# Performance work log

Measured on AMD Instinct MI355X. Metric: run time of the kernel, lower is better.

## Reference

```python
import jax, jax.numpy as jnp
import numpy as np

EPS_MASK = 1e-9   # module fills masked scores with eps, NOT -inf
LN_EPS = 1e-5

def _layer_norm(x, g, b):
    mu = jnp.mean(x, axis=-1, keepdims=True)
    var = jnp.mean(jnp.square(x - mu), axis=-1, keepdims=True)
    return (x - mu) * jax.lax.rsqrt(var + LN_EPS) * g + b

def _mha(q_in, k_in, v_in, wq, bq, wk, bk, wv, bv, wo, bo, mask, nhead):
    B, Sq, D = q_in.shape
    dk = D // nhead
    def proj(x, w, b):
        y = x @ w + b                                   # [B,S,D]
        return y.reshape(B, -1, nhead, dk).transpose(0, 2, 1, 3)  # [B,h,S,dk]
    q, k, v = proj(q_in, wq, bq), proj(k_in, wk, bk), proj(v_in, wv, bv)
    scores = jnp.einsum('bhqd,bhkd->bhqk', q, k) / np.sqrt(dk).astype(q.dtype)
    if mask is not None:
        scores = jnp.where(mask[:, None, :, :] == 0, jnp.asarray(EPS_MASK, scores.dtype), scores)
    p = jax.nn.softmax(scores, axis=-1)                 # dropout = identity (eval)
    x = jnp.einsum('bhqk,bhkd->bhqd', p, v)
    x = x.transpose(0, 2, 1, 3).reshape(B, Sq, D)
    return x @ wo + bo

def _forward_post(tgt, memory, tgt_pos, memory_pos, tgt_mask, memory_mask, p):
    nhead = 8
    # self-attention (q=k=tgt+pos, v=tgt)
    q = tgt + tgt_pos
    sa = _mha(q, q, tgt, p['sa_wq'], p['sa_bq'], p['sa_wk'], p['sa_bk'],
              p['sa_wv'], p['sa_bv'], p['sa_wo'], p['sa_bo'], tgt_mask, nhead)
    tgt = _layer_norm(tgt + sa, p['ln1_g'], p['ln1_b'])
    # cross-attention (q=tgt+tgt_pos, k=memory+memory_pos, v=memory)
    mq = tgt + tgt_pos
    mk = memory + memory_pos
    ca = _mha(mq, mk, memory, p['ca_wq'], p['ca_bq'], p['ca_wk'], p['ca_bk'],
              p['ca_wv'], p['ca_bv'], p['ca_wo'], p['ca_bo'], memory_mask, nhead)
    tgt = _layer_norm(tgt + ca, p['ln2_g'], p['ln2_b'])
    # FFN
    h = jax.nn.relu(tgt @ p['mlp_w1'] + p['mlp_b1'])
    ff = h @ p['mlp_w2'] + p['mlp_b2']
    return _layer_norm(tgt + ff, p['ln3_g'], p['ln3_b'])

def setup_inputs() -> dict:
    key = jax.random.key(0)
    B, S, M, D, H = 4, 1024, 1024, 512, 2048
    ks = iter(jax.random.split(key, 40))
    d = {
        'tgt': jax.random.normal(next(ks), (B, S, D), jnp.float32),
        'memory': jax.random.normal(next(ks), (B, M, D), jnp.float32),
        'tgt_pos': jax.random.normal(next(ks), (B, S, D), jnp.float32),
        'memory_pos': jax.random.normal(next(ks), (B, M, D), jnp.float32),
        'tgt_mask': jax.random.randint(next(ks), (B, S, S), 0, 2, jnp.int32),
        'memory_mask': jax.random.randint(next(ks), (B, S, M), 0, 2, jnp.int32),
    }
    for pre in ('sa', 'ca'):
        for nm in ('q', 'k', 'v', 'o'):
            d[f'{pre}_w{nm}'] = jax.random.normal(next(ks), (D, D), jnp.float32) * 0.02
            d[f'{pre}_b{nm}'] = jnp.zeros((D,), jnp.float32)
    for i in (1, 2, 3):
        d[f'ln{i}_g'] = jnp.ones((D,), jnp.float32)
        d[f'ln{i}_b'] = jnp.zeros((D,), jnp.float32)
    d['mlp_w1'] = jax.random.normal(next(ks), (D, H), jnp.float32) * 0.02
    d['mlp_b1'] = jnp.zeros((H,), jnp.float32)
    d['mlp_w2'] = jax.random.normal(next(ks), (H, D), jnp.float32) * 0.02
    d['mlp_b2'] = jnp.zeros((D,), jnp.float32)
    return d

def reference(tgt, memory, tgt_pos, memory_pos, tgt_mask, memory_mask,
              sa_wq, sa_bq, sa_wk, sa_bk, sa_wv, sa_bv, sa_wo, sa_bo,
              ca_wq, ca_bq, ca_wk, ca_bk, ca_wv, ca_bv, ca_wo, ca_bo,
              ln1_g, ln1_b, ln2_g, ln2_b, ln3_g, ln3_b,
              mlp_w1, mlp_b1, mlp_w2, mlp_b2):
    p = dict(sa_wq=sa_wq, sa_bq=sa_bq, sa_wk=sa_wk, sa_bk=sa_bk, sa_wv=sa_wv,
             sa_bv=sa_bv, sa_wo=sa_wo, sa_bo=sa_bo, ca_wq=ca_wq, ca_bq=ca_bq,
             ca_wk=ca_wk, ca_bk=ca_bk, ca_wv=ca_wv, ca_bv=ca_bv, ca_wo=ca_wo,
             ca_bo=ca_bo, ln1_g=ln1_g, ln1_b=ln1_b, ln2_g=ln2_g, ln2_b=ln2_b,
             ln3_g=ln3_g, ln3_b=ln3_b, mlp_w1=mlp_w1, mlp_b1=mlp_b1,
             mlp_w2=mlp_w2, mlp_b2=mlp_b2)
    return _forward_post(tgt, memory, tgt_pos, memory_pos, tgt_mask, memory_mask, p)
```

## Files before the change

kernel.cpp:

```cpp
#include <hip/hip_runtime.h>
#include <stdint.h>

typedef unsigned int u32;
typedef unsigned long long u64;
typedef unsigned short u16;
typedef __attribute__((ext_vector_type(8))) __bf16 bf16x8;
typedef __attribute__((ext_vector_type(4))) float f32x4;

#define DEV __device__ __forceinline__

DEV u16 f2bf(float f) {
    u32 x = __builtin_bit_cast(u32, f);
    u32 r = (x + 0x7FFFu + ((x >> 16) & 1u)) >> 16;
    return (u16)r;
}

DEV float bf2f(u16 x) {
    u32 u = (u32)x << 16;
    return __builtin_bit_cast(float, u);
}

DEV void unp8(uint4 u, float* f) {
    f[0] = bf2f((u16)u.x); f[1] = bf2f((u16)(u.x >> 16));
    f[2] = bf2f((u16)u.y); f[3] = bf2f((u16)(u.y >> 16));
    f[4] = bf2f((u16)u.z); f[5] = bf2f((u16)(u.z >> 16));
    f[6] = bf2f((u16)u.w); f[7] = bf2f((u16)(u.w >> 16));
}

DEV bf16x8 ldg8(const u16* p) {
    return __builtin_bit_cast(bf16x8, *(const uint4*)p);
}

DEV u32 pk2(float a, float b) {
    return (u32)f2bf(a) | ((u32)f2bf(b) << 16);
}

DEV void g2l16(const u16* g, u16* l) {
    __builtin_amdgcn_global_load_lds(
        (const __attribute__((address_space(1))) u32*)g,
        (__attribute__((address_space(3))) u32*)l, 16, 0, 0);
}

DEV f32x4 mfma16(bf16x8 a, bf16x8 b, f32x4 c) {
    return __builtin_amdgcn_mfma_f32_16x16x32_bf16(a, b, c, 0, 0, 0);
}

struct ProArgs {
    const float* w[10];
    u16* wtbase;
    const float4 *tgt, *tpos, *mem, *mpos;
    ushort4 *qin, *tgtb, *memb, *mkb, *tposb;
    const int4 *m1, *m2;
    u32 *o1, *o2;
};
__global__ __launch_bounds__(256) void prologue_kernel(ProArgs a) {
    const int bx = blockIdx.x, t = threadIdx.x;
    if (bx < 10240) {
        int z = bx >> 10, bxx = bx & 1023;
        int Kd = (z == 9) ? 2048 : 512;
        int Nd = (z == 8) ? 2048 : 512;
        size_t off = (z < 8) ? (size_t)z * 262144
                             : (z == 8 ? (size_t)2097152 : (size_t)3145728);
        u16* out = a.wtbase + off;
        int nx = Nd / 32;
        int txile = bxx % nx, tyile = bxx / nx;
        if (tyile >= Kd / 32) return;
        const float* w = a.w[z];
        __shared__ float tl[32][33];
        int tx = t & 31, ty = t >> 5;
#pragma unroll
        for (int j = 0; j < 4; ++j)
            tl[ty + j * 8][tx] = w[(size_t)(tyile * 32 + ty + j * 8) * Nd + txile * 32 + tx];
        __syncthreads();
#pragma unroll
        for (int j = 0; j < 4; ++j)
            out[(size_t)(txile * 32 + ty + j * 8) * Kd + tyile * 32 + tx] = f2bf(tl[tx][ty + j * 8]);
    } else if (bx < 12288) {
        int i = (bx - 10240) * 256 + t;
        float4 tt = a.tgt[i], p = a.tpos[i], m = a.mem[i], mp = a.mpos[i];
        a.qin[i]  = make_ushort4(f2bf(tt.x + p.x), f2bf(tt.y + p.y), f2bf(tt.z + p.z), f2bf(tt.w + p.w));
        a.tgtb[i] = make_ushort4(f2bf(tt.x), f2bf(tt.y), f2bf(tt.z), f2bf(tt.w));
        a.memb[i] = make_ushort4(f2bf(m.x), f2bf(m.y), f2bf(m.z), f2bf(m.w));
        a.mkb[i]  = make_ushort4(f2bf(m.x + mp.x), f2bf(m.y + mp.y), f2bf(m.z + mp.z), f2bf(m.w + mp.w));
        a.tposb[i]= make_ushort4(f2bf(p.x), f2bf(p.y), f2bf(p.z), f2bf(p.w));
    } else {
        int i = (bx - 12288) * 256 + t;
        const int n8 = 524288;
        bool first = i < n8;
        int idx = first ? i : i - n8;
        const int4* src = first ? a.m1 : a.m2;
        int4 x = src[idx * 2], y = src[idx * 2 + 1];
        u32 by = (u32)(x.x != 0) | ((u32)(x.y != 0) << 1) | ((u32)(x.z != 0) << 2) |
                 ((u32)(x.w != 0) << 3) | ((u32)(y.x != 0) << 4) | ((u32)(y.y != 0) << 5) |
                 ((u32)(y.z != 0) << 6) | ((u32)(y.w != 0) << 7);
        u32 w = by | (__shfl_down(by, 1) << 8) | (__shfl_down(by, 2) << 16) |
                (__shfl_down(by, 3) << 24);
        if ((t & 3) == 0) (first ? a.o1 : a.o2)[idx >> 2] = w;
    }
}

struct GemmSet {
    const u16* A; const u16* W; const float* bias; void* out;
    float oscale; int epi; int k0; int klen;
};
struct GemmArgs5 { GemmSet s[5]; };

template <int BM, int BN>
__global__ __launch_bounds__(256) void gemm_kernel(GemmArgs5 args, int M, int N, int Kd) {
    constexpr int MF = BM / 32, NF = BN / 32;
    const GemmSet gs = args.s[blockIdx.z];
    const u16* __restrict__ A = gs.A;
    const u16* __restrict__ W = gs.W;
    const int t = threadIdx.x;
    const int lane = t & 63;
    const int g = lane >> 4, r16 = lane & 15;
    const int wave = t >> 6;
    const int wm = wave >> 1, wn = wave & 1;
    const int nwg = gridDim.x * gridDim.y;
    const int fid = blockIdx.y * gridDim.x + blockIdx.x;
    const int qq = nwg >> 3;
    const int lid = (fid & 7) * qq + (fid >> 3);
    const int m0 = (lid / gridDim.x) * BM, n0 = (lid % gridDim.x) * BN;

    __shared__ __align__(16) u16 As[BM * 64];
    __shared__ __align__(16) u16 Bs[BN * 64];

    f32x4 acc[MF][NF];
#pragma unroll
    for (int m = 0; m < MF; ++m)
#pragma unroll
        for (int n = 0; n < NF; ++n) acc[m][n] = f32x4{0.f, 0.f, 0.f, 0.f};

    const int kend = gs.k0 + gs.klen;
    for (int kk = gs.k0; kk < kend; kk += 64) {
        __syncthreads();
#pragma unroll
        for (int i = 0; i < BM / 32; ++i) {
            int cid = t + i * 256, row = cid >> 3, c = cid & 7;
            g2l16(A + (size_t)(m0 + row) * Kd + kk + ((c ^ (row & 7)) << 3), &As[cid << 3]);
        }
#pragma unroll
        for (int i = 0; i < BN / 32; ++i) {
            int cid = t + i * 256, row = cid >> 3, c = cid & 7;
            g2l16(W + (size_t)(n0 + row) * Kd + kk + ((c ^ (row & 7)) << 3), &Bs[cid << 3]);
        }
        __syncthreads();
#pragma unroll
        for (int ks = 0; ks < 2; ++ks) {
            bf16x8 af[MF], bfr[NF];
#pragma unroll
            for (int m = 0; m < MF; ++m) {
                int row = wm * (MF * 16) + m * 16 + r16;
                af[m] = *(const bf16x8*)&As[(row << 6) + (((ks * 4 + g) ^ (row & 7)) << 3)];
            }
#pragma unroll
            for (int n = 0; n < NF; ++n) {
                int row = wn * (NF * 16) + n * 16 + r16;
                bfr[n] = *(const bf16x8*)&Bs[(row << 6) + (((ks * 4 + g) ^ (row & 7)) << 3)];
            }
#pragma unroll
            for (int m = 0; m < MF; ++m)
#pragma unroll
                for (int n = 0; n < NF; ++n)
                    acc[m][n] = mfma16(af[m], bfr[n], acc[m][n]);
        }
    }
    const int epi = gs.epi;
#pragma unroll
    for (int m = 0; m < MF; ++m) {
        int row0 = m0 + wm * (MF * 16) + m * 16 + g * 4;
#pragma unroll
        for (int n = 0; n < NF; ++n) {
            int col = n0 + wn * (NF * 16) + n * 16 + r16;
            float bv = gs.bias ? gs.bias[col] : 0.f;
            float v[4];
#pragma unroll
            for (int r = 0; r < 4; ++r) v[r] = (acc[m][n][r] + bv) * gs.oscale;
            if (epi == 1) {
#pragma unroll
                for (int r = 0; r < 4; ++r) v[r] = fmaxf(v[r], 0.f);
            }
            if (epi == 3) {
                int bb = row0 >> 10, s = row0 & 1023;
                u16* o = (u16*)gs.out +
                         ((size_t)(bb * 8 + (col >> 6)) * 64 + (col & 63)) * 1024 + s;
                *(ushort4*)o = make_ushort4(f2bf(v[0]), f2bf(v[1]), f2bf(v[2]), f2bf(v[3]));
            } else {
                u16* o = (u16*)gs.out;
#pragma unroll
                for (int r = 0; r < 4; ++r) o[(size_t)(row0 + r) * N + col] = f2bf(v[r]);
            }
        }
    }
}

__global__ __launch_bounds__(512, 4) void attn_part_kernel(
    const u16* __restrict__ Q, const u16* __restrict__ K,
    const u16* __restrict__ VT, const u32* __restrict__ mb,
    u16* __restrict__ OP, float2* __restrict__ ML) {
    constexpr int Lq = 1024, Lk = 1024, NCH = 8;
    const int t = threadIdx.x, lane = t & 63, wave = t >> 6;
    const int g = lane >> 4, r16 = lane & 15;
    const int h = blockIdx.y;
    const int b = blockIdx.z >> 1, p = blockIdx.z & 1;
    const int bh = b * 8 + h;
    const int q0 = blockIdx.x * 128 + wave * 16;
    const int kc0 = p * (Lk >> 1);

    __shared__ __align__(16) u16 Ks[2][64][64];
    __shared__ __align__(16) u16 Vs[2][64][64];
    __shared__ __align__(16) u16 Pl[8][16][72];

    const size_t qrow = (size_t)b * Lq + q0 + r16;
    const u16* qp = Q + qrow * 512 + h * 64 + g * 8;
    bf16x8 qb0 = ldg8(qp), qb1 = ldg8(qp + 32);
    const u32* mrow = mb + qrow * (Lk >> 5);

    const int sid = t & 255;
    const bool isK = t < 256;
    const int s1 = sid, s2 = sid + 256;
    const int r1 = s1 >> 3, c1 = s1 & 7;
    const int r2 = s2 >> 3, c2 = s2 & 7;
    const u16 *sgA, *sgB;
    if (isK) {
        const u16* kbase = K + (size_t)b * Lk * 512 + h * 64;
        sgA = kbase + (size_t)(kc0 + r1) * 512 + ((c1 ^ (r1 & 7)) << 3);
        sgB = kbase + (size_t)(kc0 + r2) * 512 + ((c2 ^ (r2 & 7)) << 3);
    } else {
        const u16* vbase = VT + (size_t)bh * 64 * Lk + kc0;
        sgA = vbase + (size_t)r1 * Lk + ((c1 ^ (r1 & 7)) << 3);
        sgB = vbase + (size_t)r2 * Lk + ((c2 ^ (r2 & 7)) << 3);
    }
    const size_t adv = isK ? (size_t)64 * 512 : 64;
    u16* const base = isK ? &Ks[0][0][0] : &Vs[0][0][0];
    u16* const slA = base + s1 * 8;
    u16* const slB = base + s2 * 8;

    f32x4 acc[4];
#pragma unroll
    for (int dt = 0; dt < 4; ++dt) acc[dt] = f32x4{0.f, 0.f, 0.f, 0.f};
    float mrun = -INFINITY, lrun = 0.f;
    const f32x4 zf = {0.f, 0.f, 0.f, 0.f};

    g2l16(sgA, slA);
    g2l16(sgB, slB);
    __syncthreads();

#pragma unroll
    for (int c = 0; c < NCH; ++c) {
        const int buf = c & 1, nbuf = buf ^ 1;
        const int kc = kc0 + c * 64;
        if (c + 1 < NCH) {
            g2l16(sgA + (size_t)(c + 1) * adv, slA + nbuf * 4096);
            g2l16(sgB + (size_t)(c + 1) * adv, slB + nbuf * 4096);
        }
        const u16* kb = &Ks[buf][0][0];
        const u16* vb = &Vs[buf][0][0];
        f32x4 s[4];
#pragma unroll
        for (int j = 0; j < 4; ++j) {
            int row = j * 16 + r16;
            bf16x8 ka0 = *(const bf16x8*)(kb + row * 64 + ((g ^ (row & 7)) << 3));
            bf16x8 ka1 = *(const bf16x8*)(kb + row * 64 + (((4 + g) ^ (row & 7)) << 3));
            s[j] = mfma16(ka0, qb0, zf);
            s[j] = mfma16(ka1, qb1, s[j]);
        }
        u32 mw0 = mrow[kc >> 5], mw1 = mrow[(kc >> 5) + 1];
        float sv[16];
#pragma unroll
        for (int j = 0; j < 4; ++j) {
            u32 w = (j < 2) ? mw0 : mw1;
            int bbase = (16 * j) & 31;
#pragma unroll
            for (int r = 0; r < 4; ++r) {
                int bit = bbase + g * 4 + r;
                sv[4 * j + r] = ((w >> bit) & 1) ? s[j][r] : 1e-9f;
            }
        }
        float tm = fmaxf(fmaxf(fmaxf(sv[0], sv[1]), fmaxf(sv[2], sv[3])),
                         fmaxf(fmaxf(sv[4], sv[5]), fmaxf(sv[6], sv[7])));
        float tm2 = fmaxf(fmaxf(fmaxf(sv[8], sv[9]), fmaxf(sv[10], sv[11])),
                          fmaxf(fmaxf(sv[12], sv[13]), fmaxf(sv[14], sv[15])));
        tm = fmaxf(tm, tm2);
        tm = fmaxf(tm, __shfl_xor(tm, 16));
        tm = fmaxf(tm, __shfl_xor(tm, 32));
        if (!__all(tm <= mrun + 8.f)) {
            float mn = fmaxf(mrun, tm);
            float alpha = __expf(mrun - mn);
            mrun = mn;
            lrun *= alpha;
#pragma unroll
            for (int r = 0; r < 4; ++r) {
                float ar = __shfl(alpha, g * 4 + r);
#pragma unroll
                for (int dt = 0; dt < 4; ++dt) acc[dt][r] *= ar;
            }
        }
        float ts = 0.f;
#pragma unroll
        for (int j = 0; j < 16; ++j) { sv[j] = __expf(sv[j] - mrun); ts += sv[j]; }
        ts += __shfl_xor(ts, 16);
        ts += __shfl_xor(ts, 32);
        lrun += ts;

#pragma unroll
        for (int j = 0; j < 4; ++j) {
            uint2 u;
            u.x = pk2(sv[4 * j], sv[4 * j + 1]);
            u.y = pk2(sv[4 * j + 2], sv[4 * j + 3]);
            *(uint2*)&Pl[wave][r16][16 * j + g * 4] = u;
        }
        bf16x8 pf0 = *(const bf16x8*)&Pl[wave][r16][g * 8];
        bf16x8 pf1 = *(const bf16x8*)&Pl[wave][r16][32 + g * 8];
#pragma unroll
        for (int dt = 0; dt < 4; ++dt) {
            int row = dt * 16 + r16;
            bf16x8 vf0 = *(const bf16x8*)(vb + row * 64 + ((g ^ (row & 7)) << 3));
            bf16x8 vf1 = *(const bf16x8*)(vb + row * 64 + (((4 + g) ^ (row & 7)) << 3));
            acc[dt] = mfma16(pf0, vf0, acc[dt]);
            acc[dt] = mfma16(pf1, vf1, acc[dt]);
        }
        __syncthreads();
    }

    if (lane < 16)
        ML[(size_t)p * 32768 + (size_t)bh * 1024 + q0 + lane] = make_float2(mrun, lrun);
    const size_t obase = (size_t)p * 2097152 + ((size_t)bh * 1024 + q0) * 64;
#pragma unroll
    for (int dt = 0; dt < 4; ++dt)
#pragma unroll
        for (int r = 0; r < 4; ++r)
            OP[obase + (size_t)(g * 4 + r) * 64 + dt * 16 + r16] = f2bf(acc[dt][r]);
}

__global__ __launch_bounds__(256) void attn_combine_kernel(
    const u16* __restrict__ OP, const float2* __restrict__ ML, u16* __restrict__ O) {
    int gid = blockIdx.x * 256 + threadIdx.x;
    int row = gid >> 3, seg = gid & 7;
    size_t idx = (size_t)row * 64 + seg * 8;
    float2 ml0 = ML[row], ml1 = ML[32768 + row];
    float M = fmaxf(ml0.x, ml1.x);
    float w0 = __expf(ml0.x - M), w1 = __expf(ml1.x - M);
    float rden = 1.f / (ml0.y * w0 + ml1.y * w1);
    w0 *= rden; w1 *= rden;
    float a[8], b[8];
    unp8(*(const uint4*)(OP + idx), a);
    unp8(*(const uint4*)(OP + 2097152 + idx), b);
    int bh = row >> 10, q = row & 1023;
    int bb = bh >> 3, h = bh & 7;
    u16* o = O + ((size_t)(bb * 1024 + q)) * 512 + h * 64 + seg * 8;
    uint4 r;
    r.x = pk2(a[0] * w0 + b[0] * w1, a[1] * w0 + b[1] * w1);
    r.y = pk2(a[2] * w0 + b[2] * w1, a[3] * w0 + b[3] * w1);
    r.z = pk2(a[4] * w0 + b[4] * w1, a[5] * w0 + b[5] * w1);
    r.w = pk2(a[6] * w0 + b[6] * w1, a[7] * w0 + b[7] * w1);
    *(uint4*)o = r;
}

template <int MODE>
__global__ __launch_bounds__(256) void ln_kernel(
    const u16* __restrict__ a, const u16* __restrict__ b1, const u16* __restrict__ b2,
    const float* __restrict__ gam, const float* __restrict__ bet,
    const u16* __restrict__ pos,
    u16* __restrict__ yb, u16* __restrict__ qb, float* __restrict__ yf) {
    const int lane = threadIdx.x & 63;
    const int row = blockIdx.x * 4 + (threadIdx.x >> 6);
    const size_t base = (size_t)row * 512 + lane * 8;
    float av[8], bv[8], cv[8];
    unp8(*(const uint4*)(a + base), av);
    unp8(*(const uint4*)(b1 + base), bv);
    unp8(*(const uint4*)(b2 + base), cv);
    float x[8];
#pragma unroll
    for (int j = 0; j < 8; ++j) x[j] = av[j] + bv[j] + cv[j];
    float s1 = 0.f, s2 = 0.f;
#pragma unroll
    for (int j = 0; j < 8; ++j) { s1 += x[j]; s2 += x[j] * x[j]; }
#pragma unroll
    for (int d = 1; d < 64; d <<= 1) { s1 += __shfl_xor(s1, d); s2 += __shfl_xor(s2, d); }
    float mean = s1 * (1.f / 512.f);
    float var = s2 * (1.f / 512.f) - mean * mean;
    float rs = rsqrtf(var + 1e-5f);
    float4 gv0 = ((const float4*)(gam + lane * 8))[0];
    float4 gv1 = ((const float4*)(gam + lane * 8))[1];
    float4 be0 = ((const float4*)(bet + lane * 8))[0];
    float4 be1 = ((const float4*)(bet + lane * 8))[1];
    float gg[8] = {gv0.x, gv0.y, gv0.z, gv0.w, gv1.x, gv1.y, gv1.z, gv1.w};
    float bb[8] = {be0.x, be0.y, be0.z, be0.w, be1.x, be1.y, be1.z, be1.w};
    float y[8];
#pragma unroll
    for (int j = 0; j < 8; ++j) y[j] = (x[j] - mean) * rs * gg[j] + bb[j];
    if (MODE == 2) {
        ((float4*)(yf + base))[0] = make_float4(y[0], y[1], y[2], y[3]);
        ((float4*)(yf + base))[1] = make_float4(y[4], y[5], y[6], y[7]);
        return;
    }
    uint4 r;
    r.x = pk2(y[0], y[1]); r.y = pk2(y[2], y[3]);
    r.z = pk2(y[4], y[5]); r.w = pk2(y[6], y[7]);
    *(uint4*)(yb + base) = r;
    if (MODE == 0) {
        float pv[8];
        unp8(*(const uint4*)(pos + base), pv);
        uint4 q;
        q.x = pk2(y[0] + pv[0], y[1] + pv[1]);
        q.y = pk2(y[2] + pv[2], y[3] + pv[3]);
        q.z = pk2(y[4] + pv[4], y[5] + pv[5]);
        q.w = pk2(y[6] + pv[6], y[7] + pv[7]);
        *(uint4*)(qb + base) = q;
    }
}

extern "C" void kernel_launch(void* const* d_in, const int* in_sizes, int n_in,
                              void* d_out, int out_size, void* d_ws, size_t ws_size,
                              hipStream_t stream) {
    (void)in_sizes; (void)n_in; (void)out_size; (void)ws_size;
    const float* tgt      = (const float*)d_in[0];
    const float* memory   = (const float*)d_in[1];
    const float* tgt_pos  = (const float*)d_in[2];
    const float* mem_pos  = (const float*)d_in[3];
    const int*   tgt_mask = (const int*)d_in[4];
    const int*   mem_mask = (const int*)d_in[5];
    const float* sa_b[4] = {(const float*)d_in[7], (const float*)d_in[9],
                            (const float*)d_in[11], (const float*)d_in[13]};
    const float* ca_b[4] = {(const float*)d_in[15], (const float*)d_in[17],
                            (const float*)d_in[19], (const float*)d_in[21]};
    const float* ln1_g = (const float*)d_in[22]; const float* ln1_b = (const float*)d_in[23];
    const float* ln2_g = (const float*)d_in[24]; const float* ln2_b = (const float*)d_in[25];
    const float* ln3_g = (const float*)d_in[26]; const float* ln3_b = (const float*)d_in[27];
    const float* mlp_b1 = (const float*)d_in[29];
    const float* mlp_b2 = (const float*)d_in[31];

    const size_t MiB = 1024 * 1024;
    char* ws = (char*)d_ws;
    u16*  WT  = (u16*)(ws + 0);
    u32*  MBS = (u32*)(ws + 8 * MiB);
    u32*  MBC = (u32*)(ws + 8 * MiB + 512 * 1024);
    u16*  QIN = (u16*)(ws + 9 * MiB);
    u16*  TGTB= (u16*)(ws + 13 * MiB);
    u16*  MEMB= (u16*)(ws + 17 * MiB);
    u16*  MKB = (u16*)(ws + 21 * MiB);
    u16*  QM  = (u16*)(ws + 25 * MiB);
    u16*  KMS = (u16*)(ws + 29 * MiB);
    u16*  KMC = (u16*)(ws + 33 * MiB);
    u16*  VTS = (u16*)(ws + 37 * MiB);
    u16*  VTC = (u16*)(ws + 41 * MiB);
    u16*  ATNB= (u16*)(ws + 45 * MiB);
    u16*  P1B = (u16*)(ws + 49 * MiB);
    u16*  X1B = (u16*)(ws + 53 * MiB);
    u16*  MQB = (u16*)(ws + 57 * MiB);
    u16*  X2B = (u16*)(ws + 61 * MiB);
    u16*  TPB = (u16*)(ws + 65 * MiB);
    u16*  P2B = (u16*)(ws + 69 * MiB);
    u16*  FFH = (u16*)(ws + 9 * MiB);
    u16*  OPB = (u16*)(ws + 96 * MiB);
    float2* MLB = (float2*)(ws + 120 * MiB);

    u16* wt[10];
    for (int z = 0; z < 8; ++z) wt[z] = WT + (size_t)z * 262144;
    wt[8] = WT + 2097152;
    wt[9] = WT + 3145728;

    ProArgs pa;
    pa.w[0] = (const float*)d_in[6];  pa.w[1] = (const float*)d_in[8];
    pa.w[2] = (const float*)d_in[10]; pa.w[3] = (const float*)d_in[12];
    pa.w[4] = (const float*)d_in[14]; pa.w[5] = (const float*)d_in[16];
    pa.w[6] = (const float*)d_in[18]; pa.w[7] = (const float*)d_in[20];
    pa.w[8] = (const float*)d_in[28]; pa.w[9] = (const float*)d_in[30];
    pa.wtbase = WT;
    pa.tgt = (const float4*)tgt; pa.tpos = (const float4*)tgt_pos;
    pa.mem = (const float4*)memory; pa.mpos = (const float4*)mem_pos;
    pa.qin = (ushort4*)QIN; pa.tgtb = (ushort4*)TGTB;
    pa.memb = (ushort4*)MEMB; pa.mkb = (ushort4*)MKB;
    pa.tposb = (ushort4*)TPB;
    pa.m1 = (const int4*)tgt_mask; pa.m2 = (const int4*)mem_mask;
    pa.o1 = MBS; pa.o2 = MBC;
    prologue_kernel<<<16384, 256, 0, stream>>>(pa);

    GemmArgs5 ga;
    ga.s[0] = {QIN,  wt[0], sa_b[0], QM,  0.125f, 0, 0, 512};
    ga.s[1] = {QIN,  wt[1], sa_b[1], KMS, 1.f,    0, 0, 512};
    ga.s[2] = {TGTB, wt[2], sa_b[2], VTS, 1.f,    3, 0, 512};
    ga.s[3] = {MKB,  wt[5], ca_b[1], KMC, 1.f,    0, 0, 512};
    ga.s[4] = {MEMB, wt[6], ca_b[2], VTC, 1.f,    3, 0, 512};
    gemm_kernel<128, 64><<<dim3(8, 32, 5), 256, 0, stream>>>(ga, 4096, 512, 512);
    attn_part_kernel<<<dim3(8, 8, 8), 512, 0, stream>>>(QM, KMS, VTS, MBS, OPB, MLB);
    attn_combine_kernel<<<1024, 256, 0, stream>>>(OPB, MLB, ATNB);
    ga.s[0] = {ATNB, wt[3], sa_b[3], P1B, 1.f, 0, 0,   256};
    ga.s[1] = {ATNB, wt[3], nullptr, P2B, 1.f, 0, 256, 256};
    ga.s[2] = ga.s[0]; ga.s[3] = ga.s[0]; ga.s[4] = ga.s[0];
    gemm_kernel<64, 64><<<dim3(8, 64, 2), 256, 0, stream>>>(ga, 4096, 512, 512);
    ln_kernel<0><<<1024, 256, 0, stream>>>(TGTB, P1B, P2B, ln1_g, ln1_b, TPB, X1B, MQB, nullptr);

    ga.s[0] = {MQB, wt[4], ca_b[0], QM, 0.125f, 0, 0, 512};
    ga.s[1] = ga.s[0]; ga.s[2] = ga.s[0]; ga.s[3] = ga.s[0]; ga.s[4] = ga.s[0];
    gemm_kernel<64, 64><<<dim3(8, 64, 1), 256, 0, stream>>>(ga, 4096, 512, 512);
    attn_part_kernel<<<dim3(8, 8, 8), 512, 0, stream>>>(QM, KMC, VTC, MBC, OPB, MLB);
    attn_combine_kernel<<<1024, 256, 0, stream>>>(OPB, MLB, ATNB);
    ga.s[0] = {ATNB, wt[7], ca_b[3], P1B, 1.f, 0, 0,   256};
    ga.s[1] = {ATNB, wt[7], nullptr, P2B, 1.f, 0, 256, 256};
    ga.s[2] = ga.s[0]; ga.s[3] = ga.s[0]; ga.s[4] = ga.s[0];
    gemm_kernel<64, 64><<<dim3(8, 64, 2), 256, 0, stream>>>(ga, 4096, 512, 512);
    ln_kernel<1><<<1024, 256, 0, stream>>>(X1B, P1B, P2B, ln2_g, ln2_b, nullptr, X2B, nullptr, nullptr);

    ga.s[0] = {X2B, wt[8], mlp_b1, FFH, 1.f, 1, 0, 512};
    ga.s[1] = ga.s[0]; ga.s[2] = ga.s[0]; ga.s[3] = ga.s[0]; ga.s[4] = ga.s[0];
    gemm_kernel<128, 64><<<dim3(32, 32, 1), 256, 0, stream>>>(ga, 4096, 2048, 512);
    ga.s[0] = {FFH, wt[9], mlp_b2, P1B, 1.f, 0, 0,    1024};
    ga.s[1] = {FFH, wt[9], nullptr, P2B, 1.f, 0, 1024, 1024};
    ga.s[2] = ga.s[0]; ga.s[3] = ga.s[0]; ga.s[4] = ga.s[0];
    gemm_kernel<64, 64><<<dim3(8, 64, 2), 256, 0, stream>>>(ga, 4096, 512, 2048);
    ln_kernel<2><<<1024, 256, 0, stream>>>(X2B, P1B, P2B, ln3_g, ln3_b, nullptr,
                                           nullptr, nullptr, (float*)d_out);
}
```

Before: 161.9 us.

## Fuse split-KV attention combine into output-projection GEMM A-tile load

```diff
diff --git a/kernel.cpp b/kernel.cpp
--- a/kernel.cpp
+++ b/kernel.cpp
@@ -102,6 +102,7 @@
 struct GemmSet {
     const u16* A; const u16* W; const float* bias; void* out;
     float oscale; int epi; int k0; int klen;
+    const u16* A2; const float2* ml;
 };
 struct GemmArgs5 { GemmSet s[5]; };
 
@@ -134,10 +135,35 @@
     const int kend = gs.k0 + gs.klen;
     for (int kk = gs.k0; kk < kend; kk += 64) {
         __syncthreads();
-#pragma unroll
-        for (int i = 0; i < BM / 32; ++i) {
-            int cid = t + i * 256, row = cid >> 3, c = cid & 7;
-            g2l16(A + (size_t)(m0 + row) * Kd + kk + ((c ^ (row & 7)) << 3), &As[cid << 3]);
+        if (gs.A2) {
+            const int bb = m0 >> 10, q0t = m0 & 1023;
+            const int h = kk >> 6;
+#pragma unroll
+            for (int i = 0; i < BM / 32; ++i) {
+                int cid = t + i * 256, row = cid >> 3, c = cid & 7;
+                size_t mlidx = (size_t)(bb * 8 + h) * 1024 + q0t + row;
+                float2 ml0 = gs.ml[mlidx], ml1 = gs.ml[32768 + mlidx];
+                float Mx = fmaxf(ml0.x, ml1.x);
+                float w0 = __expf(ml0.x - Mx), w1 = __expf(ml1.x - Mx);
+                float rd = 1.f / (ml0.y * w0 + ml1.y * w1);
+                w0 *= rd; w1 *= rd;
+                size_t oidx = mlidx * 64 + ((c ^ (row & 7)) << 3);
+                float a0[8], a1[8];
+                unp8(*(const uint4*)(A + oidx), a0);
+                unp8(*(const uint4*)(gs.A2 + oidx), a1);
+                uint4 r;
+                r.x = pk2(a0[0] * w0 + a1[0] * w1, a0[1] * w0 + a1[1] * w1);
+                r.y = pk2(a0[2] * w0 + a1[2] * w1, a0[3] * w0 + a1[3] * w1);
+                r.z = pk2(a0[4] * w0 + a1[4] * w1, a0[5] * w0 + a1[5] * w1);
+                r.w = pk2(a0[6] * w0 + a1[6] * w1, a0[7] * w0 + a1[7] * w1);
+                *(uint4*)&As[cid << 3] = r;
+            }
+        } else {
+#pragma unroll
+            for (int i = 0; i < BM / 32; ++i) {
+                int cid = t + i * 256, row = cid >> 3, c = cid & 7;
+                g2l16(A + (size_t)(m0 + row) * Kd + kk + ((c ^ (row & 7)) << 3), &As[cid << 3]);
+            }
         }
 #pragma unroll
         for (int i = 0; i < BN / 32; ++i) {
@@ -201,10 +227,10 @@
     constexpr int Lq = 1024, Lk = 1024, NCH = 8;
     const int t = threadIdx.x, lane = t & 63, wave = t >> 6;
     const int g = lane >> 4, r16 = lane & 15;
-    const int h = blockIdx.y;
-    const int b = blockIdx.z >> 1, p = blockIdx.z & 1;
+    const int h = blockIdx.x;
+    const int b = blockIdx.y >> 1, p = blockIdx.y & 1;
     const int bh = b * 8 + h;
-    const int q0 = blockIdx.x * 128 + wave * 16;
+    const int q0 = blockIdx.z * 128 + wave * 16;
     const int kc0 = p * (Lk >> 1);
 
     __shared__ __align__(16) u16 Ks[2][64][64];
@@ -331,30 +357,6 @@
 #pragma unroll
         for (int r = 0; r < 4; ++r)
             OP[obase + (size_t)(g * 4 + r) * 64 + dt * 16 + r16] = f2bf(acc[dt][r]);
-}
-
-__global__ __launch_bounds__(256) void attn_combine_kernel(
-    const u16* __restrict__ OP, const float2* __restrict__ ML, u16* __restrict__ O) {
-    int gid = blockIdx.x * 256 + threadIdx.x;
-    int row = gid >> 3, seg = gid & 7;
-    size_t idx = (size_t)row * 64 + seg * 8;
-    float2 ml0 = ML[row], ml1 = ML[32768 + row];
-    float M = fmaxf(ml0.x, ml1.x);
-    float w0 = __expf(ml0.x - M), w1 = __expf(ml1.x - M);
-    float rden = 1.f / (ml0.y * w0 + ml1.y * w1);
-    w0 *= rden; w1 *= rden;
-    float a[8], b[8];
-    unp8(*(const uint4*)(OP + idx), a);
-    unp8(*(const uint4*)(OP + 2097152 + idx), b);
-    int bh = row >> 10, q = row & 1023;
-    int bb = bh >> 3, h = bh & 7;
-    u16* o = O + ((size_t)(bb * 1024 + q)) * 512 + h * 64 + seg * 8;
-    uint4 r;
-    r.x = pk2(a[0] * w0 + b[0] * w1, a[1] * w0 + b[1] * w1);
-    r.y = pk2(a[2] * w0 + b[2] * w1, a[3] * w0 + b[3] * w1);
-    r.z = pk2(a[4] * w0 + b[4] * w1, a[5] * w0 + b[5] * w1);
-    r.w = pk2(a[6] * w0 + b[6] * w1, a[7] * w0 + b[7] * w1);
-    *(uint4*)o = r;
 }
 
 template <int MODE>
@@ -445,7 +447,6 @@
     u16*  KMC = (u16*)(ws + 33 * MiB);
     u16*  VTS = (u16*)(ws + 37 * MiB);
     u16*  VTC = (u16*)(ws + 41 * MiB);
-    u16*  ATNB= (u16*)(ws + 45 * MiB);
     u16*  P1B = (u16*)(ws + 49 * MiB);
     u16*  X1B = (u16*)(ws + 53 * MiB);
     u16*  MQB = (u16*)(ws + 57 * MiB);
@@ -478,36 +479,34 @@
     prologue_kernel<<<16384, 256, 0, stream>>>(pa);
 
     GemmArgs5 ga;
-    ga.s[0] = {QIN,  wt[0], sa_b[0], QM,  0.125f, 0, 0, 512};
-    ga.s[1] = {QIN,  wt[1], sa_b[1], KMS, 1.f,    0, 0, 512};
-    ga.s[2] = {TGTB, wt[2], sa_b[2], VTS, 1.f,    3, 0, 512};
-    ga.s[3] = {MKB,  wt[5], ca_b[1], KMC, 1.f,    0, 0, 512};
-    ga.s[4] = {MEMB, wt[6], ca_b[2], VTC, 1.f,    3, 0, 512};
+    ga.s[0] = {QIN,  wt[0], sa_b[0], QM,  0.125f, 0, 0, 512, nullptr, nullptr};
+    ga.s[1] = {QIN,  wt[1], sa_b[1], KMS, 1.f,    0, 0, 512, nullptr, nullptr};
+    ga.s[2] = {TGTB, wt[2], sa_b[2], VTS, 1.f,    3, 0, 512, nullptr, nullptr};
+    ga.s[3] = {MKB,  wt[5], ca_b[1], KMC, 1.f,    0, 0, 512, nullptr, nullptr};
+    ga.s[4] = {MEMB, wt[6], ca_b[2], VTC, 1.f,    3, 0, 512, nullptr, nullptr};
     gemm_kernel<128, 64><<<dim3(8, 32, 5), 256, 0, stream>>>(ga, 4096, 512, 512);
     attn_part_kernel<<<dim3(8, 8, 8), 512, 0, stream>>>(QM, KMS, VTS, MBS, OPB, MLB);
-    attn_combine_kernel<<<1024, 256, 0, stream>>>(OPB, MLB, ATNB);
-    ga.s[0] = {ATNB, wt[3], sa_b[3], P1B, 1.f, 0, 0,   256};
-    ga.s[1] = {ATNB, wt[3], nullptr, P2B, 1.f, 0, 256, 256};
+    ga.s[0] = {OPB, wt[3], sa_b[3], P1B, 1.f, 0, 0,   256, OPB + 2097152, MLB};
+    ga.s[1] = {OPB, wt[3], nullptr, P2B, 1.f, 0, 256, 256, OPB + 2097152, MLB};
     ga.s[2] = ga.s[0]; ga.s[3] = ga.s[0]; ga.s[4] = ga.s[0];
     gemm_kernel<64, 64><<<dim3(8, 64, 2), 256, 0, stream>>>(ga, 4096, 512, 512);
     ln_kernel<0><<<1024, 256, 0, stream>>>(TGTB, P1B, P2B, ln1_g, ln1_b, TPB, X1B, MQB, nullptr);
 
-    ga.s[0] = {MQB, wt[4], ca_b[0], QM, 0.125f, 0, 0, 512};
+    ga.s[0] = {MQB, wt[4], ca_b[0], QM, 0.125f, 0, 0, 512, nullptr, nullptr};
     ga.s[1] = ga.s[0]; ga.s[2] = ga.s[0]; ga.s[3] = ga.s[0]; ga.s[4] = ga.s[0];
     gemm_kernel<64, 64><<<dim3(8, 64, 1), 256, 0, stream>>>(ga, 4096, 512, 512);
     attn_part_kernel<<<dim3(8, 8, 8), 512, 0, stream>>>(QM, KMC, VTC, MBC, OPB, MLB);
-    attn_combine_kernel<<<1024, 256, 0, stream>>>(OPB, MLB, ATNB);
-    ga.s[0] = {ATNB, wt[7], ca_b[3], P1B, 1.f, 0, 0,   256};
-    ga.s[1] = {ATNB, wt[7], nullptr, P2B, 1.f, 0, 256, 256};
+    ga.s[0] = {OPB, wt[7], ca_b[3], P1B, 1.f, 0, 0,   256, OPB + 2097152, MLB};
+    ga.s[1] = {OPB, wt[7], nullptr, P2B, 1.f, 0, 256, 256, OPB + 2097152, MLB};
     ga.s[2] = ga.s[0]; ga.s[3] = ga.s[0]; ga.s[4] = ga.s[0];
     gemm_kernel<64, 64><<<dim3(8, 64, 2), 256, 0, stream>>>(ga, 4096, 512, 512);
     ln_kernel<1><<<1024, 256, 0, stream>>>(X1B, P1B, P2B, ln2_g, ln2_b, nullptr, X2B, nullptr, nullptr);
 
-    ga.s[0] = {X2B, wt[8], mlp_b1, FFH, 1.f, 1, 0, 512};
+    ga.s[0] = {X2B, wt[8], mlp_b1, FFH, 1.f, 1, 0, 512, nullptr, nullptr};
     ga.s[1] = ga.s[0]; ga.s[2] = ga.s[0]; ga.s[3] = ga.s[0]; ga.s[4] = ga.s[0];
     gemm_kernel<128, 64><<<dim3(32, 32, 1), 256, 0, stream>>>(ga, 4096, 2048, 512);
-    ga.s[0] = {FFH, wt[9], mlp_b2, P1B, 1.f, 0, 0,    1024};
-    ga.s[1] = {FFH, wt[9], nullptr, P2B, 1.f, 0, 1024, 1024};
+    ga.s[0] = {FFH, wt[9], mlp_b2, P1B, 1.f, 0, 0,    1024, nullptr, nullptr};
+    ga.s[1] = {FFH, wt[9], nullptr, P2B, 1.f, 0, 1024, 1024, nullptr, nullptr};
     ga.s[2] = ga.s[0]; ga.s[3] = ga.s[0]; ga.s[4] = ga.s[0];
     gemm_kernel<64, 64><<<dim3(8, 64, 2), 256, 0, stream>>>(ga, 4096, 512, 2048);
     ln_kernel<2><<<1024, 256, 0, stream>>>(X2B, P1B, P2B, ln3_g, ln3_b, nullptr,
```

After: 164.1 us. About the same (+1.4%).
